# Performance work log

Hardware: AMD Instinct MI355X
Metric: run time of the kernel (lower is better)

The kernel has to match this reference:

```python
import jax, jax.numpy as jnp
import numpy as np

S, B, H, NH = 2048, 2, 1024, 16
DH = H // NH

def setup_inputs() -> dict:
    key = jax.random.key(0)
    ks = jax.random.split(key, 4)
    x = jax.random.normal(ks[0], (S, B, H), dtype=jnp.float32)
    attention_mask = jnp.ones((B, 1, S, S), dtype=bool)
    rotary_pos_emb = jax.random.uniform(ks[1], (S, 1, 1, DH), dtype=jnp.float32)
    Wqkv = jax.random.normal(ks[2], (H, 3 * H), dtype=jnp.float32) * (1.0 / np.sqrt(H))
    bqkv = jnp.zeros((3 * H,), dtype=jnp.float32)
    Wproj = jax.random.normal(ks[3], (H, H), dtype=jnp.float32) * (1.0 / np.sqrt(H))
    bproj = jnp.zeros((H,), dtype=jnp.float32)
    return {"x": x, "attention_mask": attention_mask, "rotary_pos_emb": rotary_pos_emb,
            "Wqkv": Wqkv, "bqkv": bqkv, "Wproj": Wproj, "bproj": bproj}

def reference(x, attention_mask, rotary_pos_emb, Wqkv, bqkv, Wproj, bproj):
    s, b, h = x.shape
    dh = h // NH
    # QKV projection; per-head layout [s,b,NH,3*dh] then split (matches view+chunk)
    qkv = (x @ Wqkv + bqkv).reshape(s, b, NH, 3 * dh)
    q, k, v = jnp.split(qkv, 3, axis=-1)  # each [s,b,NH,dh]
    # RoPE (non-interleaved, rot_dim == head_dim)
    cos = jnp.cos(rotary_pos_emb)  # [s,1,1,dh]
    sin = jnp.sin(rotary_pos_emb)
    def rope(t):
        t1, t2 = jnp.split(t, 2, axis=-1)
        return t * cos + jnp.concatenate((-t2, t1), axis=-1) * sin
    q = rope(q)
    k = rope(k)
    scale = 1.0 / np.sqrt(dh).astype(np.float32)
    # scores: [b,NH,t,s]
    scores = jnp.einsum('tbhd,sbhd->bhts', q, k) * scale
    scores = jnp.where(attention_mask, scores, jnp.float32(-1e9))
    attn = jax.nn.softmax(scores, axis=-1)
    out = jnp.einsum('bhts,sbhd->tbhd', attn, v).reshape(s, b, h)
    return out @ Wproj + bproj
```

## Files before the change

### kernel.cpp

```cpp
#include <hip/hip_runtime.h>
#include <hip/hip_bf16.h>

typedef __attribute__((ext_vector_type(8))) short bf16x8;
typedef __attribute__((ext_vector_type(4))) float f32x4;
typedef __attribute__((ext_vector_type(16))) float f32x16;
typedef __attribute__((ext_vector_type(4))) unsigned short u16x4;

#define S_LEN 2048
#define BATCH 2
#define NHEAD 16
#define DHEAD 64
#define HD    1024
#define MROWS 4096
#define NQKV  3072
#define NBH   32
#define KSPLIT 2
#define KSEG  (S_LEN / KSPLIT)


static __device__ __forceinline__ unsigned short f2bf(float f) {
  union { float f; unsigned u; } v; v.f = f;
  unsigned r = v.u + 0x7FFFu + ((v.u >> 16) & 1u);
  return (unsigned short)(r >> 16);
}
static __device__ __forceinline__ float bf2f(unsigned short h) {
  union { unsigned u; float f; } v; v.u = ((unsigned)h) << 16;
  return v.f;
}
static __device__ __forceinline__ unsigned cvt_pk(float a, float b) {
  unsigned r;
  asm("v_cvt_pk_bf16_f32 %0, %1, %2" : "=v"(r) : "v"(a), "v"(b));
  return r;
}
static __device__ __forceinline__ float exp2_hw(float x) {
  float r;
  asm("v_exp_f32 %0, %1" : "=v"(r) : "v"(x));
  return r;
}

static __device__ __forceinline__ void gl_lds16(const void* g, void* l) {
  __builtin_amdgcn_global_load_lds(
      (__attribute__((address_space(1))) void*)g,
      (__attribute__((address_space(3))) void*)l, 16, 0, 0);
}

__global__ void k_cvt(const float* __restrict__ x, unsigned short* __restrict__ Xfm) {
  __shared__ float ltile[64][36];
  int mt = blockIdx.x, kp = blockIdx.y;
  int t = threadIdx.x;
  int r = t >> 3, c4 = t & 7;
  const float* src = x + (size_t)(mt * 64 + r) * HD + kp * 32 + c4 * 4;
  float4 v0 = *reinterpret_cast<const float4*>(src);
  float4 v1 = *reinterpret_cast<const float4*>(src + (size_t)32 * HD);
  *reinterpret_cast<float4*>(&ltile[r][c4 * 4]) = v0;
  *reinterpret_cast<float4*>(&ltile[r + 32][c4 * 4]) = v1;
  __syncthreads();
  int rowin = ((t >> 6) << 4) + (t & 15), ch = (t >> 4) & 3;
  bf16x8 o;
#pragma unroll
  for (int e = 0; e < 8; ++e) o[e] = (short)f2bf(ltile[rowin][ch * 8 + e]);
  *reinterpret_cast<bf16x8*>(Xfm + (((size_t)mt * 32 + kp) * 256 + t) * 8) = o;
}

__global__ void k_transw(const float* __restrict__ W, unsigned short* __restrict__ Wt,
                         int K, int N) {
  __shared__ unsigned short tile[64][72];
  int n0 = blockIdx.x * 64, k0 = blockIdx.y * 64;
  int t = threadIdx.x;
  int r  = t >> 2;
  int c4 = (t & 3) * 16;
  const float* src = W + (size_t)(k0 + r) * N + n0 + c4;
#pragma unroll
  for (int j = 0; j < 16; j += 4) {
    float4 v = *reinterpret_cast<const float4*>(src + j);
    tile[r][c4 + j + 0] = f2bf(v.x);
    tile[r][c4 + j + 1] = f2bf(v.y);
    tile[r][c4 + j + 2] = f2bf(v.z);
    tile[r][c4 + j + 3] = f2bf(v.w);
  }
  __syncthreads();
  int rowin = ((t >> 6) << 4) + (t & 15), ch = (t >> 4) & 3;
  int nt = blockIdx.x;
  int KP = K >> 5;
#pragma unroll
  for (int p = 0; p < 2; ++p) {
    bf16x8 o;
#pragma unroll
    for (int e = 0; e < 8; ++e) o[e] = (short)tile[p * 32 + ch * 8 + e][rowin];
    *reinterpret_cast<bf16x8*>(Wt + (((size_t)nt * KP + (k0 >> 5) + p) * 256 + t) * 8) = o;
  }
}

template <int OUT_BF16, int BN>
__global__ void __launch_bounds__(256)
k_gemm(const unsigned short* __restrict__ A, const unsigned short* __restrict__ Bt,
       const float* __restrict__ bias, void* __restrict__ Cout, int M, int N, int K) {
  constexpr int NF = BN / 32;
  __shared__ unsigned short As[128 * 32];
  __shared__ unsigned short Bs[BN * 32];
  int t = threadIdx.x;
  int lane = t & 63;
  int w = t >> 6;
  int g = lane >> 4, i = lane & 15;
  int wr = w >> 1, wc = w & 1;
  int bx = blockIdx.x, by = blockIdx.y;

  f32x4 acc[4][NF] = {};

  const size_t tstride = (size_t)K * 64;
  const unsigned short* a_s0 = A  + (size_t)(2 * by) * tstride + t * 8;
  const unsigned short* a_s1 = a_s0 + tstride;
  const unsigned short* b_s0 = Bt + (size_t)(bx * (BN / 64)) * tstride + t * 8;
  const unsigned short* b_s1 = b_s0 + tstride;
  unsigned short* a_d0 = &As[t * 8];
  unsigned short* a_d1 = &As[(256 + t) * 8];
  unsigned short* b_d0 = &Bs[t * 8];
  unsigned short* b_d1 = &Bs[(256 + t) * 8];

  for (int kt = 0; kt < K; kt += 32) {
    size_t koff = (size_t)kt * 64;
    __syncthreads();
    gl_lds16(a_s0 + koff, a_d0);
    gl_lds16(a_s1 + koff, a_d1);
    gl_lds16(b_s0 + koff, b_d0);
    if constexpr (BN == 128) gl_lds16(b_s1 + koff, b_d1);
    __syncthreads();

    bf16x8 af[4], bf[NF];
#pragma unroll
    for (int m = 0; m < 4; ++m)
      af[m] = *reinterpret_cast<const bf16x8*>(&As[(wr * 256 + m * 64 + lane) * 8]);
#pragma unroll
    for (int n = 0; n < NF; ++n)
      bf[n] = *reinterpret_cast<const bf16x8*>(&Bs[((wc * NF + n) * 64 + lane) * 8]);
#pragma unroll
    for (int m = 0; m < 4; ++m)
#pragma unroll
      for (int n = 0; n < NF; ++n)
        acc[m][n] = __builtin_amdgcn_mfma_f32_16x16x32_bf16(af[m], bf[n], acc[m][n], 0, 0, 0);
  }

  int crow0 = by * 128 + wr * 64;
  int ccol0 = bx * BN + wc * (BN / 2);
#pragma unroll
  for (int n = 0; n < NF; ++n) {
    int col = ccol0 + n * 16 + i;
    float bv = bias[col];
#pragma unroll
    for (int m = 0; m < 4; ++m) {
#pragma unroll
      for (int r = 0; r < 4; ++r) {
        int row = crow0 + m * 16 + g * 4 + r;
        float v = acc[m][n][r] + bv;
        if (OUT_BF16)
          reinterpret_cast<unsigned short*>(Cout)[(size_t)row * N + col] = f2bf(v);
        else
          reinterpret_cast<float*>(Cout)[(size_t)row * N + col] = v;
      }
    }
  }
}

__global__ void k_rope(const unsigned short* __restrict__ QKV, const float* __restrict__ rot,
                       unsigned short* __restrict__ Qg, unsigned short* __restrict__ Kg,
                       unsigned short* __restrict__ Vg) {
  __shared__ unsigned short vtile[32][72];
  int s0 = blockIdx.x * 32;
  int bh = blockIdx.y;
  int b = bh >> 4, nh = bh & 15;
  int t = threadIdx.x;
  int c  = t & 31;
  int hi = (t >> 5) & 1;
  int ks = t >> 6;
  int d0 = ks * 16 + hi * 8;
  int s = s0 + c;
  const unsigned short* base = QKV + ((size_t)s * BATCH + b) * NQKV + nh * 192;

  float cs[8], sn[8];
#pragma unroll
  for (int j = 0; j < 8; j += 4) {
    float4 rv = *reinterpret_cast<const float4*>(rot + (size_t)s * DHEAD + d0 + j);
    cs[j + 0] = cosf(rv.x); sn[j + 0] = sinf(rv.x);
    cs[j + 1] = cosf(rv.y); sn[j + 1] = sinf(rv.y);
    cs[j + 2] = cosf(rv.z); sn[j + 2] = sinf(rv.z);
    cs[j + 3] = cosf(rv.w); sn[j + 3] = sinf(rv.w);
  }
  float sgn = (d0 < 32) ? -1.f : 1.f;
  bf16x8 qv = *reinterpret_cast<const bf16x8*>(base + d0);
  bf16x8 qp = *reinterpret_cast<const bf16x8*>(base + (d0 ^ 32));
  bf16x8 kv = *reinterpret_cast<const bf16x8*>(base + 64 + d0);
  bf16x8 kp = *reinterpret_cast<const bf16x8*>(base + 64 + (d0 ^ 32));
  bf16x8 qo, ko;
#pragma unroll
  for (int j = 0; j < 8; ++j) {
    float q = bf2f((unsigned short)qv[j]) * cs[j] + sgn * bf2f((unsigned short)qp[j]) * sn[j];
    float k = bf2f((unsigned short)kv[j]) * cs[j] + sgn * bf2f((unsigned short)kp[j]) * sn[j];
    qo[j] = (short)f2bf(q * 0.18033688f);
    ko[j] = (short)f2bf(k);
  }
  size_t blk = ((size_t)bh * (S_LEN / 32) + (s0 >> 5)) * 2048;
  *reinterpret_cast<bf16x8*>(Qg + blk + t * 8) = qo;
  *reinterpret_cast<bf16x8*>(Kg + blk + t * 8) = ko;

  bf16x8 vv = *reinterpret_cast<const bf16x8*>(base + 128 + d0);
  *reinterpret_cast<bf16x8*>(&vtile[c][d0]) = vv;
  __syncthreads();
  int vbr = t >> 7, h = (t >> 6) & 1, hi2 = (t >> 5) & 1, cc = t & 31;
  int d = 32 * h + cc;
  bf16x8 vo;
#pragma unroll
  for (int j = 0; j < 8; ++j) vo[j] = (short)vtile[vbr * 16 + hi2 * 8 + j][d];
  size_t vblk = ((size_t)bh * (S_LEN / 16) + (s0 >> 4) + vbr) * 1024;
  *reinterpret_cast<bf16x8*>(Vg + vblk + (t & 127) * 8) = vo;
}

static __device__ __forceinline__ void sm_pv(const f32x16& sc, const bf16x8* vfr,
                                             float& l_acc, f32x16& o0, f32x16& o1) {
  float p[16];
#pragma unroll
  for (int r = 0; r < 16; ++r) p[r] = exp2_hw(sc[r]);
  float s0 = (p[0] + p[1]) + (p[2] + p[3]);
  float s1 = (p[4] + p[5]) + (p[6] + p[7]);
  float s2 = (p[8] + p[9]) + (p[10] + p[11]);
  float s3 = (p[12] + p[13]) + (p[14] + p[15]);
  l_acc += (s0 + s1) + (s2 + s3);
#pragma unroll
  for (int ksl = 0; ksl < 2; ++ksl) {
    unsigned A0 = cvt_pk(p[8 * ksl + 0], p[8 * ksl + 1]);
    unsigned A1 = cvt_pk(p[8 * ksl + 2], p[8 * ksl + 3]);
    unsigned A2 = cvt_pk(p[8 * ksl + 4], p[8 * ksl + 5]);
    unsigned A3 = cvt_pk(p[8 * ksl + 6], p[8 * ksl + 7]);
    asm volatile("v_permlane32_swap_b32 %0, %1" : "+v"(A0), "+v"(A2));
    asm volatile("v_permlane32_swap_b32 %0, %1" : "+v"(A1), "+v"(A3));
    union { unsigned u[4]; bf16x8 v; } pa;
    pa.u[0] = A0; pa.u[1] = A1; pa.u[2] = A2; pa.u[3] = A3;
    __builtin_amdgcn_s_setprio(1);
    o0 = __builtin_amdgcn_mfma_f32_32x32x16_bf16(pa.v, vfr[2 * ksl + 0], o0, 0, 0, 0);
    o1 = __builtin_amdgcn_mfma_f32_32x32x16_bf16(pa.v, vfr[2 * ksl + 1], o1, 0, 0, 0);
    __builtin_amdgcn_s_setprio(0);
  }
}

__global__ void __launch_bounds__(256, 2)
k_flash(const unsigned short* __restrict__ Qg, const unsigned short* __restrict__ Kg,
        const unsigned short* __restrict__ Vg, unsigned short* __restrict__ Opart,
        float* __restrict__ Lpart) {
  __shared__ unsigned short kv_lds[2 * 8192];
  int bh = blockIdx.x, qt = blockIdx.y, kv = blockIdx.z;
  int t = threadIdx.x, lane = t & 63;
  int c = lane & 31, hi = lane >> 5;

  int q0 = qt * 128 + (t >> 6) * 32;
  int kv0 = kv * KSEG;
  const unsigned short* Qb = Qg + (size_t)bh * S_LEN * DHEAD + (size_t)q0 * DHEAD;
  const unsigned short* Kb = Kg + (size_t)bh * S_LEN * DHEAD;
  const unsigned short* Vb = Vg + (size_t)bh * S_LEN * DHEAD;

  bf16x8 qf[4];
#pragma unroll
  for (int ks = 0; ks < 4; ++ks)
    qf[ks] = *reinterpret_cast<const bf16x8*>(Qb + ((size_t)ks * 64 + lane) * 8);

#define STAGE(kt, bufi) do {                                                   \
    const unsigned short* _ks = Kb + (size_t)(kt) * DHEAD;                     \
    const unsigned short* _vs = Vb + (size_t)(kt) * DHEAD;                     \
    unsigned short* _kd = &kv_lds[(bufi) * 8192];                              \
    unsigned short* _vd = _kd + 4096;                                          \
    gl_lds16(_ks + t * 8, _kd + t * 8);                                        \
    gl_lds16(_ks + (t + 256) * 8, _kd + (t + 256) * 8);                        \
    gl_lds16(_vs + t * 8, _vd + t * 8);                                        \
    gl_lds16(_vs + (t + 256) * 8, _vd + (t + 256) * 8);                        \
  } while (0)

  f32x16 o0 = {}, o1 = {};
  float l_acc = 0.f;
  int cur = 0;

  STAGE(kv0, 0);
  for (int kt = kv0; kt < kv0 + KSEG; kt += 64) {
    __syncthreads();
    int nxt = kv0 + (((kt - kv0) + 64) & (KSEG - 1));
    STAGE(nxt, cur ^ 1);

    const unsigned short* kbuf = &kv_lds[cur * 8192];
    const unsigned short* vbuf = kbuf + 4096;

    f32x16 scA = {}, scB = {};
    __builtin_amdgcn_s_setprio(1);
#pragma unroll
    for (int ks = 0; ks < 4; ++ks) {
      bf16x8 kf = *reinterpret_cast<const bf16x8*>(kbuf + (ks * 64 + lane) * 8);
      scA = __builtin_amdgcn_mfma_f32_32x32x16_bf16(kf, qf[ks], scA, 0, 0, 0);
    }
#pragma unroll
    for (int ks = 0; ks < 4; ++ks) {
      bf16x8 kf = *reinterpret_cast<const bf16x8*>(kbuf + (256 + ks * 64 + lane) * 8);
      scB = __builtin_amdgcn_mfma_f32_32x32x16_bf16(kf, qf[ks], scB, 0, 0, 0);
    }
    __builtin_amdgcn_s_setprio(0);

    bf16x8 va[4], vb[4];
#pragma unroll
    for (int g = 0; g < 2; ++g) {
      va[2 * g + 0] = *reinterpret_cast<const bf16x8*>(vbuf + (g * 128 + lane) * 8);
      va[2 * g + 1] = *reinterpret_cast<const bf16x8*>(vbuf + (g * 128 + 64 + lane) * 8);
      vb[2 * g + 0] = *reinterpret_cast<const bf16x8*>(vbuf + ((g + 2) * 128 + lane) * 8);
      vb[2 * g + 1] = *reinterpret_cast<const bf16x8*>(vbuf + ((g + 2) * 128 + 64 + lane) * 8);
    }

    sm_pv(scA, va, l_acc, o0, o1);
    sm_pv(scB, vb, l_acc, o0, o1);
    cur ^= 1;
  }
#undef STAGE

  float l_tot = l_acc + __shfl_xor(l_acc, 32, 64);

  unsigned short* Op = Opart + ((size_t)kv * NBH + bh) * S_LEN * DHEAD;
  if (hi == 0) Lpart[((size_t)kv * NBH + bh) * S_LEN + q0 + c] = l_tot;
#pragma unroll
  for (int r = 0; r < 16; ++r) {
    int crow = (r & 3) + 8 * (r >> 2) + 4 * hi;
    size_t rowoff = (size_t)(q0 + crow) * DHEAD;
    Op[rowoff + c]      = f2bf(o0[r]);
    Op[rowoff + 32 + c] = f2bf(o1[r]);
  }
}

__global__ void k_reduce(const unsigned short* __restrict__ Op, const float* __restrict__ Lp,
                         unsigned short* __restrict__ Afm) {
  __shared__ unsigned short lds[64][72];
  const int kvO = NBH * S_LEN * DHEAD;
  const int kvL = NBH * S_LEN;
  int mt = blockIdx.x, nh = blockIdx.y;
  int t = threadIdx.x;
  int lq = (t >> 3) & 31, gd = t & 7;
  int qg = mt * 32 + lq;

  bf16x8 gr[4];
#pragma unroll
  for (int kvb = 0; kvb < 4; ++kvb) {
    int kv = kvb >> 1, b = kvb & 1;
    gr[kvb] = *reinterpret_cast<const bf16x8*>(
        Op + (size_t)kv * kvO + ((size_t)(b * 16 + nh) * S_LEN + qg) * DHEAD + gd * 8);
  }
#pragma unroll
  for (int b = 0; b < 2; ++b) {
    size_t li = (size_t)(b * 16 + nh) * S_LEN + qg;
    float inv = 1.0f / (Lp[li] + Lp[kvL + li]);
    bf16x8 o;
#pragma unroll
    for (int e = 0; e < 8; ++e)
      o[e] = (short)f2bf((bf2f((unsigned short)gr[b][e]) +
                          bf2f((unsigned short)gr[2 + b][e])) * inv);
    *reinterpret_cast<bf16x8*>(&lds[b * 32 + lq][gd * 8]) = o;
  }
  __syncthreads();

  int rowin = ((t >> 6) << 4) + (t & 15), ch = (t >> 4) & 3;
  int lr = (rowin & 1) * 32 + (rowin >> 1);
#pragma unroll
  for (int p = 0; p < 2; ++p) {
    bf16x8 o = *reinterpret_cast<const bf16x8*>(&lds[lr][p * 32 + ch * 8]);
    *reinterpret_cast<bf16x8*>(Afm + (((size_t)mt * 32 + nh * 2 + p) * 256 + t) * 8) = o;
  }
}

extern "C" void kernel_launch(void* const* d_in, const int* in_sizes, int n_in,
                              void* d_out, int out_size, void* d_ws, size_t ws_size,
                              hipStream_t stream) {
  const float* x     = (const float*)d_in[0];
  const float* rot   = (const float*)d_in[2];
  const float* Wqkv  = (const float*)d_in[3];
  const float* bqkv  = (const float*)d_in[4];
  const float* Wproj = (const float*)d_in[5];
  const float* bproj = (const float*)d_in[6];
  float* out = (float*)d_out;

  char* ws = (char*)d_ws;
  unsigned short* xb   = (unsigned short*)(ws);
  unsigned short* Wqt  = (unsigned short*)(ws + 8388608);
  unsigned short* Wpt  = (unsigned short*)(ws + 14680064);
  unsigned short* QKV  = (unsigned short*)(ws + 16777216);
  unsigned short* Qs   = (unsigned short*)(ws + 41943040);
  unsigned short* Kst  = (unsigned short*)(ws + 50331648);
  unsigned short* Vtt  = (unsigned short*)(ws + 58720256);
  unsigned short* Opart = (unsigned short*)(ws + 16777216);
  float*          Lpart = (float*)(ws + 33554432);
  unsigned short* attn  = xb;

  k_cvt<<<dim3(MROWS / 64, HD / 32), 256, 0, stream>>>(x, xb);
  k_transw<<<dim3(NQKV / 64, HD / 64), 256, 0, stream>>>(Wqkv, Wqt, HD, NQKV);
  k_transw<<<dim3(HD / 64, HD / 64), 256, 0, stream>>>(Wproj, Wpt, HD, HD);
  k_gemm<1, 128><<<dim3(NQKV / 128, MROWS / 128), 256, 0, stream>>>(xb, Wqt, bqkv, QKV,
                                                                    MROWS, NQKV, HD);
  k_rope<<<dim3(S_LEN / 32, BATCH * NHEAD), 256, 0, stream>>>(QKV, rot, Qs, Kst, Vtt);
  k_flash<<<dim3(NBH, S_LEN / 128, KSPLIT), 256, 0, stream>>>(Qs, Kst, Vtt, Opart, Lpart);
  k_reduce<<<dim3(MROWS / 64, NHEAD), 256, 0, stream>>>(Opart, Lpart, attn);
  k_gemm<0, 64><<<dim3(HD / 64, MROWS / 128), 256, 0, stream>>>(attn, Wpt, bproj, out,
                                                                MROWS, HD, HD);
}
```

Before: 134.8 us.

## Double GEMM K-step to 64 and remap workgroups across XCDs

The GEMM kernel now stages 64 K-elements per iteration instead of 32, so it does half as many barrier pairs and issues more MFMAs per synchronization. It also remaps the linear workgroup id with a stride-8 permutation, so consecutive tiles land on the same XCD and share L2 reuse of A/B panels. LDS usage doubles, which may reduce occupancy. The remap assumes the total workgroup count is divisible by 8.

After: 137.4 us. No clear change (+1.9%).

```diff
diff --git a/kernel.cpp b/kernel.cpp
--- a/kernel.cpp
+++ b/kernel.cpp
@@ -96,14 +96,19 @@
 k_gemm(const unsigned short* __restrict__ A, const unsigned short* __restrict__ Bt,
        const float* __restrict__ bias, void* __restrict__ Cout, int M, int N, int K) {
   constexpr int NF = BN / 32;
-  __shared__ unsigned short As[128 * 32];
-  __shared__ unsigned short Bs[BN * 32];
+  __shared__ unsigned short As[128 * 64];
+  __shared__ unsigned short Bs[BN * 64];
   int t = threadIdx.x;
   int lane = t & 63;
   int w = t >> 6;
   int g = lane >> 4, i = lane & 15;
   int wr = w >> 1, wc = w & 1;
-  int bx = blockIdx.x, by = blockIdx.y;
+
+  int nx = gridDim.x;
+  int nwg = nx * gridDim.y;
+  int id = blockIdx.y * nx + blockIdx.x;
+  int id2 = (id & 7) * (nwg >> 3) + (id >> 3);
+  int bx = id2 % nx, by = id2 / nx;
 
   f32x4 acc[4][NF] = {};
 
@@ -112,32 +117,42 @@
   const unsigned short* a_s1 = a_s0 + tstride;
   const unsigned short* b_s0 = Bt + (size_t)(bx * (BN / 64)) * tstride + t * 8;
   const unsigned short* b_s1 = b_s0 + tstride;
-  unsigned short* a_d0 = &As[t * 8];
-  unsigned short* a_d1 = &As[(256 + t) * 8];
-  unsigned short* b_d0 = &Bs[t * 8];
-  unsigned short* b_d1 = &Bs[(256 + t) * 8];
-
-  for (int kt = 0; kt < K; kt += 32) {
+
+  for (int kt = 0; kt < K; kt += 64) {
     size_t koff = (size_t)kt * 64;
     __syncthreads();
-    gl_lds16(a_s0 + koff, a_d0);
-    gl_lds16(a_s1 + koff, a_d1);
-    gl_lds16(b_s0 + koff, b_d0);
-    if constexpr (BN == 128) gl_lds16(b_s1 + koff, b_d1);
+    gl_lds16(a_s0 + koff,        &As[t * 8]);
+    gl_lds16(a_s0 + koff + 2048, &As[(256 + t) * 8]);
+    gl_lds16(a_s1 + koff,        &As[(512 + t) * 8]);
+    gl_lds16(a_s1 + koff + 2048, &As[(768 + t) * 8]);
+    gl_lds16(b_s0 + koff,        &Bs[t * 8]);
+    gl_lds16(b_s0 + koff + 2048, &Bs[(256 + t) * 8]);
+    if constexpr (BN == 128) {
+      gl_lds16(b_s1 + koff,        &Bs[(512 + t) * 8]);
+      gl_lds16(b_s1 + koff + 2048, &Bs[(768 + t) * 8]);
+    }
     __syncthreads();
 
-    bf16x8 af[4], bf[NF];
-#pragma unroll
-    for (int m = 0; m < 4; ++m)
-      af[m] = *reinterpret_cast<const bf16x8*>(&As[(wr * 256 + m * 64 + lane) * 8]);
-#pragma unroll
-    for (int n = 0; n < NF; ++n)
-      bf[n] = *reinterpret_cast<const bf16x8*>(&Bs[((wc * NF + n) * 64 + lane) * 8]);
-#pragma unroll
-    for (int m = 0; m < 4; ++m)
-#pragma unroll
-      for (int n = 0; n < NF; ++n)
-        acc[m][n] = __builtin_amdgcn_mfma_f32_16x16x32_bf16(af[m], bf[n], acc[m][n], 0, 0, 0);
+#pragma unroll
+    for (int p = 0; p < 2; ++p) {
+      bf16x8 af[4], bf[NF];
+#pragma unroll
+      for (int m = 0; m < 4; ++m)
+        af[m] = *reinterpret_cast<const bf16x8*>(
+            &As[((wr * 2 + p) * 256 + m * 64 + lane) * 8]);
+#pragma unroll
+      for (int n = 0; n < NF; ++n) {
+        int bpanel = (BN == 128) ? (wc * 2 + p) : p;
+        int bgroup = (BN == 128) ? n : (wc * NF + n);
+        bf[n] = *reinterpret_cast<const bf16x8*>(
+            &Bs[(bpanel * 256 + bgroup * 64 + lane) * 8]);
+      }
+#pragma unroll
+      for (int m = 0; m < 4; ++m)
+#pragma unroll
+        for (int n = 0; n < NF; ++n)
+          acc[m][n] = __builtin_amdgcn_mfma_f32_16x16x32_bf16(af[m], bf[n], acc[m][n], 0, 0, 0);
+    }
   }
 
   int crow0 = by * 128 + wr * 64;
@@ -214,6 +229,7 @@
   *reinterpret_cast<bf16x8*>(Vg + vblk + (t & 127) * 8) = vo;
 }
 
+
 static __device__ __forceinline__ void sm_pv(const f32x16& sc, const bf16x8* vfr,
                                              float& l_acc, f32x16& o0, f32x16& o1) {
   float p[16];
```
